# Performance work log

Measured on AMD Instinct MI355X. Metric: run time of the kernel, lower is better.

The kernel has to match this reference:

```python
import jax, jax.numpy as jnp
import numpy as np

IN_CHANNELS = 64


def _haar_weights(in_channels: int) -> jnp.ndarray:
    # Matches torch construction: (4, 1, 2, 2), then sign flips, *0.25, tiled per channel.
    w = np.ones((4, 1, 2, 2), dtype=np.float32)
    w[1, 0, 0, 1] = -1
    w[1, 0, 1, 1] = -1
    w[2, 0, 1, 0] = -1
    w[2, 0, 1, 1] = -1
    w[3, 0, 1, 0] = -1
    w[3, 0, 0, 1] = -1
    w = w * 0.25
    w = np.concatenate([w] * in_channels, axis=0)  # (4*C, 1, 2, 2) OIHW
    return jnp.asarray(w)


def setup_inputs() -> dict:
    key = jax.random.key(0)
    B, C, H, W = 8, IN_CHANNELS, 512, 512
    inputs = jax.random.normal(key, (B, C, H, W), dtype=jnp.float32)
    weights = _haar_weights(IN_CHANNELS)
    return {"inputs": inputs, "weights": weights}


def reference(inputs, weights):
    # Forward Haar transform (reverse=False path).
    B, C, H, W = inputs.shape
    # Depthwise (grouped) 2x2 stride-2 conv: out channels = 4*C, grouped by C.
    out = jax.lax.conv_general_dilated(
        inputs, weights,
        window_strides=(2, 2), padding='VALID',
        dimension_numbers=('NCHW', 'OIHW', 'NCHW'),
        feature_group_count=C,
    )  # (B, 4*C, H/2, W/2), channel-major layout [c0:(LL,LH,HL,HH), c1:...]
    # Regroup to subband-major: (B, 4, C, h, w) -> (B, 4*C, h, w)
    h, w = H // 2, W // 2
    out = out.reshape(B, C, 4, h, w).transpose(0, 2, 1, 3, 4).reshape(B, C * 4, h, w)
    return out
```

## Files before the change

### kernel.cpp

```cpp
#include <hip/hip_runtime.h>


constexpr int B  = 8;
constexpr int C  = 64;
constexpr int H  = 512;
constexpr int W  = 512;
constexpr int HO = H / 2;
constexpr int WO = W / 2;
constexpr int W4 = WO / 4;

__global__ __launch_bounds__(256) void haar_fwd(const float* __restrict__ x,
                                                float* __restrict__ y) {
    const int total = B * C * HO * W4;
    int idx = blockIdx.x * blockDim.x + threadIdx.x;
    if (idx >= total) return;

    const int j4 = idx % W4;
    int t = idx / W4;
    const int i = t % HO;
    t /= HO;
    const int c = t % C;
    const int b = t / C;

    const float* r0 = x + (((size_t)(b * C + c) * H + 2 * i) * W + 8 * (size_t)j4);
    const float* r1 = r0 + W;
    const float4 r0a = *reinterpret_cast<const float4*>(r0);
    const float4 r0b = *reinterpret_cast<const float4*>(r0 + 4);
    const float4 r1a = *reinterpret_cast<const float4*>(r1);
    const float4 r1b = *reinterpret_cast<const float4*>(r1 + 4);

    const float a0 = r0a.x, b0 = r0a.y, a1 = r0a.z, b1 = r0a.w;
    const float a2 = r0b.x, b2 = r0b.y, a3 = r0b.z, b3 = r0b.w;
    const float c0 = r1a.x, d0 = r1a.y, c1 = r1a.z, d1 = r1a.w;
    const float c2 = r1b.x, d2 = r1b.y, c3 = r1b.z, d3 = r1b.w;

    float4 ll, k1, k2, k3;
    ll.x = 0.25f * (a0 + b0 + c0 + d0);
    ll.y = 0.25f * (a1 + b1 + c1 + d1);
    ll.z = 0.25f * (a2 + b2 + c2 + d2);
    ll.w = 0.25f * (a3 + b3 + c3 + d3);

    k1.x = 0.25f * (a0 - b0 + c0 - d0);
    k1.y = 0.25f * (a1 - b1 + c1 - d1);
    k1.z = 0.25f * (a2 - b2 + c2 - d2);
    k1.w = 0.25f * (a3 - b3 + c3 - d3);

    k2.x = 0.25f * (a0 + b0 - c0 - d0);
    k2.y = 0.25f * (a1 + b1 - c1 - d1);
    k2.z = 0.25f * (a2 + b2 - c2 - d2);
    k2.w = 0.25f * (a3 + b3 - c3 - d3);

    k3.x = 0.25f * (a0 - b0 - c0 + d0);
    k3.y = 0.25f * (a1 - b1 - c1 + d1);
    k3.z = 0.25f * (a2 - b2 - c2 + d2);
    k3.w = 0.25f * (a3 - b3 - c3 + d3);

    const size_t plane = (size_t)HO * WO;
    const size_t rowoff = (size_t)i * WO + 4 * (size_t)j4;
    float* ybase = y + ((size_t)b * 4 * C + c) * plane + rowoff;

    *reinterpret_cast<float4*>(ybase)                      = ll;
    *reinterpret_cast<float4*>(ybase + (size_t)C * plane)      = k1;
    *reinterpret_cast<float4*>(ybase + (size_t)2 * C * plane)  = k2;
    *reinterpret_cast<float4*>(ybase + (size_t)3 * C * plane)  = k3;
}

extern "C" void kernel_launch(void* const* d_in, const int* in_sizes, int n_in,
                              void* d_out, int out_size, void* d_ws, size_t ws_size,
                              hipStream_t stream) {
    const float* x = (const float*)d_in[0];
    float* y = (float*)d_out;

    const int total = B * C * HO * W4;
    const int threads = 256;
    const int blocks = (total + threads - 1) / threads;
    haar_fwd<<<blocks, threads, 0, stream>>>(x, y);
}
```

Baseline: 211.5 us.

## Use grid-stride loop with float4 loads and float2 stores per thread

```diff
diff --git a/kernel.cpp b/kernel.cpp
--- a/kernel.cpp
+++ b/kernel.cpp
@@ -7,62 +7,43 @@
 constexpr int W  = 512;
 constexpr int HO = H / 2;
 constexpr int WO = W / 2;
-constexpr int W4 = WO / 4;
+constexpr int JC = W / 4;
+constexpr int TOTAL = B * C * HO * JC;
 
 __global__ __launch_bounds__(256) void haar_fwd(const float* __restrict__ x,
                                                 float* __restrict__ y) {
-    const int total = B * C * HO * W4;
-    int idx = blockIdx.x * blockDim.x + threadIdx.x;
-    if (idx >= total) return;
+    const int stride = gridDim.x * blockDim.x;
+    const size_t plane = (size_t)HO * WO;
+    for (int idx = blockIdx.x * blockDim.x + threadIdx.x; idx < TOTAL; idx += stride) {
+        const int j = idx & (JC - 1);
+        const int i = (idx >> 7) & (HO - 1);
+        const int m = idx >> 15;
 
-    const int j4 = idx % W4;
-    int t = idx / W4;
-    const int i = t % HO;
-    t /= HO;
-    const int c = t % C;
-    const int b = t / C;
+        const float* p0 = x + ((size_t)m * H + 2 * (size_t)i) * W + 4 * (size_t)j;
+        const float4 r0 = *reinterpret_cast<const float4*>(p0);
+        const float4 r1 = *reinterpret_cast<const float4*>(p0 + W);
 
-    const float* r0 = x + (((size_t)(b * C + c) * H + 2 * i) * W + 8 * (size_t)j4);
-    const float* r1 = r0 + W;
-    const float4 r0a = *reinterpret_cast<const float4*>(r0);
-    const float4 r0b = *reinterpret_cast<const float4*>(r0 + 4);
-    const float4 r1a = *reinterpret_cast<const float4*>(r1);
-    const float4 r1b = *reinterpret_cast<const float4*>(r1 + 4);
+        const float s0 = r0.x + r0.y, d0 = r0.x - r0.y;
+        const float t0 = r0.z + r0.w, e0 = r0.z - r0.w;
+        const float s1 = r1.x + r1.y, d1 = r1.x - r1.y;
+        const float t1 = r1.z + r1.w, e1 = r1.z - r1.w;
 
-    const float a0 = r0a.x, b0 = r0a.y, a1 = r0a.z, b1 = r0a.w;
-    const float a2 = r0b.x, b2 = r0b.y, a3 = r0b.z, b3 = r0b.w;
-    const float c0 = r1a.x, d0 = r1a.y, c1 = r1a.z, d1 = r1a.w;
-    const float c2 = r1b.x, d2 = r1b.y, c3 = r1b.z, d3 = r1b.w;
+        float2 ll, k1, k2, k3;
+        ll.x = 0.25f * (s0 + s1);  ll.y = 0.25f * (t0 + t1);
+        k1.x = 0.25f * (d0 + d1);  k1.y = 0.25f * (e0 + e1);
+        k2.x = 0.25f * (s0 - s1);  k2.y = 0.25f * (t0 - t1);
+        k3.x = 0.25f * (d0 - d1);  k3.y = 0.25f * (e0 - e1);
 
-    float4 ll, k1, k2, k3;
-    ll.x = 0.25f * (a0 + b0 + c0 + d0);
-    ll.y = 0.25f * (a1 + b1 + c1 + d1);
-    ll.z = 0.25f * (a2 + b2 + c2 + d2);
-    ll.w = 0.25f * (a3 + b3 + c3 + d3);
+        const int bimg = m >> 6;
+        const int cimg = m & (C - 1);
+        float* yb = y + ((size_t)bimg * 4 * C + cimg) * plane
+                      + (size_t)i * WO + 2 * (size_t)j;
 
-    k1.x = 0.25f * (a0 - b0 + c0 - d0);
-    k1.y = 0.25f * (a1 - b1 + c1 - d1);
-    k1.z = 0.25f * (a2 - b2 + c2 - d2);
-    k1.w = 0.25f * (a3 - b3 + c3 - d3);
-
-    k2.x = 0.25f * (a0 + b0 - c0 - d0);
-    k2.y = 0.25f * (a1 + b1 - c1 - d1);
-    k2.z = 0.25f * (a2 + b2 - c2 - d2);
-    k2.w = 0.25f * (a3 + b3 - c3 - d3);
-
-    k3.x = 0.25f * (a0 - b0 - c0 + d0);
-    k3.y = 0.25f * (a1 - b1 - c1 + d1);
-    k3.z = 0.25f * (a2 - b2 - c2 + d2);
-    k3.w = 0.25f * (a3 - b3 - c3 + d3);
-
-    const size_t plane = (size_t)HO * WO;
-    const size_t rowoff = (size_t)i * WO + 4 * (size_t)j4;
-    float* ybase = y + ((size_t)b * 4 * C + c) * plane + rowoff;
-
-    *reinterpret_cast<float4*>(ybase)                      = ll;
-    *reinterpret_cast<float4*>(ybase + (size_t)C * plane)      = k1;
-    *reinterpret_cast<float4*>(ybase + (size_t)2 * C * plane)  = k2;
-    *reinterpret_cast<float4*>(ybase + (size_t)3 * C * plane)  = k3;
+        *reinterpret_cast<float2*>(yb)                         = ll;
+        *reinterpret_cast<float2*>(yb + (size_t)C * plane)     = k1;
+        *reinterpret_cast<float2*>(yb + (size_t)2 * C * plane) = k2;
+        *reinterpret_cast<float2*>(yb + (size_t)3 * C * plane) = k3;
+    }
 }
 
 extern "C" void kernel_launch(void* const* d_in, const int* in_sizes, int n_in,
@@ -71,8 +52,7 @@
     const float* x = (const float*)d_in[0];
     float* y = (float*)d_out;
 
-    const int total = B * C * HO * W4;
     const int threads = 256;
-    const int blocks = (total + threads - 1) / threads;
+    const int blocks = 2048;
     haar_fwd<<<blocks, threads, 0, stream>>>(x, y);
 }
```

Result: slower. 241.3 us (+14.1%).
